# Kernel tuning notes

Measured on AMD Instinct MI355X. Metric: run time of the kernel, lower is better.

The kernel has to match this reference:

```python
import jax, jax.numpy as jnp
import numpy as np

T, B = 64, 512
X, H, Z, A = 1024, 1024, 256, 64


def setup_inputs() -> dict:
    key = jax.random.key(0)
    ks = jax.random.split(key, 24)
    s = 0.02
    n = lambda k, shape: (jax.random.normal(k, shape, dtype=jnp.float32) * s)
    d = {
        "obs_seq": jax.random.normal(ks[0], (T, B, X), dtype=jnp.float32),
        "act_seq": jax.random.normal(ks[1], (T, B, A), dtype=jnp.float32),
        "eps": jax.random.normal(ks[2], (T, B, Z), dtype=jnp.float32),
        # Transition: aggr Linear(z+a -> h), GRUCell(h, h)
        "aggr_W": n(ks[3], (Z + A, H)), "aggr_b": jnp.zeros((H,), jnp.float32),
        "gru_Wih": n(ks[4], (H, 3 * H)), "gru_Whh": n(ks[5], (H, 3 * H)),
        "gru_bih": jnp.zeros((3 * H,), jnp.float32), "gru_bhh": jnp.zeros((3 * H,), jnp.float32),
        # z_q_dist: NormalPredictor(x+h -> hidden h -> z)
        "q_W1": n(ks[6], (X + H, H)), "q_b1": jnp.zeros((H,), jnp.float32),
        "q_Wm": n(ks[7], (H, Z)), "q_bm": jnp.zeros((Z,), jnp.float32),
        "q_Ws": n(ks[8], (H, Z)), "q_bs": jnp.zeros((Z,), jnp.float32),
        # z_p_dist: NormalPredictor(h -> hidden h -> z)
        "p_W1": n(ks[9], (H, H)), "p_b1": jnp.zeros((H,), jnp.float32),
        "p_Wm": n(ks[10], (H, Z)), "p_bm": jnp.zeros((Z,), jnp.float32),
        "p_Ws": n(ks[11], (H, Z)), "p_bs": jnp.zeros((Z,), jnp.float32),
    }
    return d


def _gru_cell(x, h, Wih, Whh, bih, bhh):
    # torch.nn.GRUCell math
    gi = x @ Wih + bih
    gh = h @ Whh + bhh
    i_r, i_z, i_n = jnp.split(gi, 3, axis=-1)
    h_r, h_z, h_n = jnp.split(gh, 3, axis=-1)
    r = jax.nn.sigmoid(i_r + h_r)
    z = jax.nn.sigmoid(i_z + h_z)
    n = jnp.tanh(i_n + r * h_n)
    return (1.0 - z) * n + z * h


def _normal_predictor(x, W1, b1, Wm, bm, Ws, bs):
    hid = jax.nn.elu(x @ W1 + b1)
    loc = hid @ Wm + bm
    scale = jax.nn.softplus(hid @ Ws + bs)
    return loc, scale


def reference(obs_seq, act_seq, eps, aggr_W, aggr_b, gru_Wih, gru_Whh, gru_bih,
              gru_bhh, q_W1, q_b1, q_Wm, q_bm, q_Ws, q_bs, p_W1, p_b1, p_Wm,
              p_bm, p_Ws, p_bs):
    batch = obs_seq.shape[1]
    h0 = jnp.zeros((batch, gru_Whh.shape[0]), dtype=obs_seq.dtype)

    def step(h, inp):
        obs, act, e = inp
        q_loc, q_scale = _normal_predictor(
            jnp.concatenate([obs, h], axis=-1), q_W1, q_b1, q_Wm, q_bm, q_Ws, q_bs)
        z_q = q_loc + q_scale * e  # rsample
        p_loc, p_scale = _normal_predictor(h, p_W1, p_b1, p_Wm, p_bm, p_Ws, p_bs)
        a = jax.nn.elu(jnp.concatenate([z_q, act], axis=-1) @ aggr_W + aggr_b)
        h_new = _gru_cell(a, h, gru_Wih, gru_Whh, gru_bih, gru_bhh)
        return h_new, (h_new, q_loc, q_scale, p_loc, p_scale, z_q)

    _, (bel, q_loc, q_scale, p_loc, p_scale, z_qs) = jax.lax.scan(
        step, h0, (obs_seq, act_seq, eps))
    beliefs = jnp.concatenate([h0[None], bel], axis=0)  # [T+1, B, H]
    return beliefs, (q_loc, q_scale), (p_loc, p_scale), z_qs
```

## Files before the change

### kernel.cpp

```cpp
#include <hip/hip_runtime.h>
#include <hip/hip_bf16.h>
#include <stdint.h>

#define TT 64
#define BB 512
#define XX 1024
#define HH 1024
#define ZZ 256
#define AA 64

typedef __bf16 bf16;
typedef bf16 bf16x8 __attribute__((ext_vector_type(8)));
typedef float f32x4 __attribute__((ext_vector_type(4)));

#define SZ_BEL ((long)(TT + 1) * BB * HH)
#define SZ_TBZ ((long)TT * BB * ZZ)
#define OFF_QL (SZ_BEL)
#define OFF_QS (OFF_QL + SZ_TBZ)
#define OFF_ZQ (OFF_QL + 4 * SZ_TBZ)

#define GLL16(g, l)                                                         \
  __builtin_amdgcn_global_load_lds(                                         \
      (__attribute__((address_space(1))) void*)(g),                         \
      (__attribute__((address_space(3))) void*)(l), 16, 0, 0)

__device__ __forceinline__ float eluf(float x) {
  return x > 0.f ? x : expf(x) - 1.f;
}
__device__ __forceinline__ float splusf(float x) {
  return fmaxf(x, 0.f) + log1pf(expf(-fabsf(x)));
}
__device__ __forceinline__ float sigf(float x) {
  return 1.f / (1.f + expf(-x));
}

struct GArgs {
  const bf16* A; const float* Af; const bf16* A2;
  long lda, lda2; int ksplit;
  const bf16* Bt;
  int M, N, K, t;
  const float *b_q1, *b_p1, *b_ghh, *b_gih;
  const float *b_qm, *b_qs, *b_pm, *b_ps, *b_ag;
  const bf16* obs_pre;
  bf16 *hid_q, *hid_p, *a_buf, *out_bf;
  float *gh, *gi, *dout;
};

template <int BM, int BN, int EPI, bool AF32>
__global__ __launch_bounds__(256) void gemm_k(GArgs g) {
  constexpr int BK = 32;
  constexpr int WTM = BM / 2, WTN = BN / 2;
  constexpr int MR = WTM / 16, NR = WTN / 16;
  constexpr int CA = BM * 4 / 256, CB = BN * 4 / 256;
  __shared__ bf16 sA[BM * BK];
  __shared__ bf16 sB[BN * BK];
  const int nbm = g.M / BM;
  const int bm = blockIdx.x % nbm, bn = blockIdx.x / nbm;
  const int m0 = bm * BM, n0 = bn * BN;
  const int tid = threadIdx.x;
  const int wid = tid >> 6, lane = tid & 63;
  const int wm = wid & 1, wn = wid >> 1;
  const int lr = lane & 15, lk = lane >> 4;

  const bf16* Ap = g.A;
  if (EPI == 2 && n0 >= 512) Ap = g.A2;

  f32x4 acc[MR][NR] = {};

  for (int k0 = 0; k0 < g.K; k0 += BK) {
    __syncthreads();
    if constexpr (AF32) {
#pragma unroll
      for (int i = 0; i < CA; i++) {
        int c = tid + i * 256, row = c >> 2, kc = c & 3;
        const float* s = g.Af + (long)(m0 + row) * g.lda + k0 + kc * 8;
        float4 v0 = *(const float4*)s;
        float4 v1 = *(const float4*)(s + 4);
        bf16x8 p;
        p[0] = (bf16)v0.x; p[1] = (bf16)v0.y; p[2] = (bf16)v0.z; p[3] = (bf16)v0.w;
        p[4] = (bf16)v1.x; p[5] = (bf16)v1.y; p[6] = (bf16)v1.z; p[7] = (bf16)v1.w;
        *(bf16x8*)&sA[c * 8] = p;
      }
    } else {
#pragma unroll
      for (int i = 0; i < CA; i++) {
        int c = tid + i * 256, row = c >> 2, kc = c & 3;
        const bf16* s;
        if (EPI == 3 && k0 >= g.ksplit)
          s = g.A2 + (long)(m0 + row) * g.lda2 + (k0 - g.ksplit) + kc * 8;
        else
          s = Ap + (long)(m0 + row) * g.lda + k0 + kc * 8;
        GLL16(s, &sA[c * 8]);
      }
    }
#pragma unroll
    for (int i = 0; i < CB; i++) {
      int c = tid + i * 256, row = c >> 2, kc = c & 3;
      GLL16(g.Bt + (long)(n0 + row) * g.K + k0 + kc * 8, &sB[c * 8]);
    }
    __syncthreads();
    bf16x8 af[MR];
#pragma unroll
    for (int mi = 0; mi < MR; mi++)
      af[mi] = *(const bf16x8*)&sA[(wm * WTM + mi * 16 + lr) * BK + lk * 8];
#pragma unroll
    for (int nj = 0; nj < NR; nj++) {
      bf16x8 bfr = *(const bf16x8*)&sB[(wn * WTN + nj * 16 + lr) * BK + lk * 8];
#pragma unroll
      for (int mi = 0; mi < MR; mi++)
        acc[mi][nj] = __builtin_amdgcn_mfma_f32_16x16x32_bf16(af[mi], bfr, acc[mi][nj], 0, 0, 0);
    }
  }

#pragma unroll
  for (int mi = 0; mi < MR; mi++) {
#pragma unroll
    for (int nj = 0; nj < NR; nj++) {
#pragma unroll
      for (int r = 0; r < 4; r++) {
        const int row = m0 + wm * WTM + mi * 16 + lk * 4 + r;
        const int col = n0 + wn * WTN + nj * 16 + lr;
        float v = acc[mi][nj][r];
        if constexpr (EPI == 0) {
          g.out_bf[(long)row * g.N + col] = (bf16)v;
        } else if constexpr (EPI == 1) {
          if (col < HH) {
            float x = v + g.b_q1[col] + (float)g.obs_pre[((long)g.t * BB + row) * HH + col];
            g.hid_q[row * HH + col] = (bf16)eluf(x);
          } else if (col < 2 * HH) {
            int j = col - HH;
            g.hid_p[row * HH + j] = (bf16)eluf(v + g.b_p1[j]);
          } else {
            int j = col - 2 * HH;
            g.gh[(long)row * 3 * HH + j] = v + g.b_ghh[j];
          }
        } else if constexpr (EPI == 2) {
          int region = col >> 8, j = col & 255;
          const float* bias = region == 0 ? g.b_qm : region == 1 ? g.b_qs
                            : region == 2 ? g.b_pm : g.b_ps;
          float x = v + bias[j];
          if (region & 1) x = splusf(x);
          g.dout[OFF_QL + (long)region * SZ_TBZ + ((long)g.t * BB + row) * ZZ + j] = x;
        } else if constexpr (EPI == 3) {
          g.a_buf[row * HH + col] = (bf16)eluf(v + g.b_ag[col]);
        } else {
          g.gi[(long)row * 3 * HH + col] = v + g.b_gih[col];
        }
      }
    }
  }
}

__global__ void transpose_cvt(const float* __restrict__ src, bf16* __restrict__ dst,
                              int K, int N, int ld, int k_off) {
  __shared__ float tile[32][33];
  const int nb = blockIdx.x * 32, kb = blockIdx.y * 32;
  const int tx = threadIdx.x, ty = threadIdx.y;
#pragma unroll
  for (int j = 0; j < 32; j += 8)
    tile[ty + j][tx] = src[(long)(kb + ty + j + k_off) * ld + nb + tx];
  __syncthreads();
#pragma unroll
  for (int j = 0; j < 32; j += 8)
    dst[(long)(nb + ty + j) * K + kb + tx] = (bf16)tile[tx][ty + j];
}

__global__ void cvt_bf16(const float* __restrict__ src, bf16* __restrict__ dst, long n) {
  long i = ((long)blockIdx.x * blockDim.x + threadIdx.x) * 4;
  if (i < n) {
    float4 v = *(const float4*)(src + i);
    dst[i] = (bf16)v.x; dst[i + 1] = (bf16)v.y;
    dst[i + 2] = (bf16)v.z; dst[i + 3] = (bf16)v.w;
  }
}

__global__ void init_k(bf16* hbf, float* dout) {
  int i = blockIdx.x * 256 + threadIdx.x;
  hbf[i] = (bf16)0.f;
  dout[i] = 0.f;
}

__global__ void zq_k(const float* __restrict__ eps, float* dout, bf16* zbf, int t) {
  long i = (long)blockIdx.x * 256 + threadIdx.x;
  long o = (long)t * BB * ZZ + i;
  float ql = dout[OFF_QL + o], qs = dout[OFF_QS + o];
  float z = ql + qs * eps[o];
  dout[OFF_ZQ + o] = z;
  zbf[i] = (bf16)z;
}

__global__ void gates_k(const float* __restrict__ gi, const float* __restrict__ gh,
                        bf16* hbf, float* dout, int t) {
  long i = (long)blockIdx.x * 256 + threadIdx.x;
  int m = (int)(i >> 10), j = (int)(i & 1023);
  long b = (long)m * 3 * HH + j;
  float r = sigf(gi[b] + gh[b]);
  float z = sigf(gi[b + HH] + gh[b + HH]);
  float nn = tanhf(gi[b + 2 * HH] + r * gh[b + 2 * HH]);
  float h = (float)hbf[i];
  float hnew = (1.f - z) * nn + z * h;
  hbf[i] = (bf16)hnew;
  dout[(long)(t + 1) * BB * HH + i] = hnew;
}

extern "C" void kernel_launch(void* const* d_in, const int* in_sizes, int n_in,
                              void* d_out, int out_size, void* d_ws, size_t ws_size,
                              hipStream_t stream) {
  const float* obs  = (const float*)d_in[0];
  const float* act  = (const float*)d_in[1];
  const float* eps  = (const float*)d_in[2];
  const float* aggrW = (const float*)d_in[3];
  const float* aggrB = (const float*)d_in[4];
  const float* gWih = (const float*)d_in[5];
  const float* gWhh = (const float*)d_in[6];
  const float* gbih = (const float*)d_in[7];
  const float* gbhh = (const float*)d_in[8];
  const float* qW1  = (const float*)d_in[9];
  const float* qb1  = (const float*)d_in[10];
  const float* qWm  = (const float*)d_in[11];
  const float* qbm  = (const float*)d_in[12];
  const float* qWs  = (const float*)d_in[13];
  const float* qbs  = (const float*)d_in[14];
  const float* pW1  = (const float*)d_in[15];
  const float* pb1  = (const float*)d_in[16];
  const float* pWm  = (const float*)d_in[17];
  const float* pbm  = (const float*)d_in[18];
  const float* pWs  = (const float*)d_in[19];
  const float* pbs  = (const float*)d_in[20];
  float* dout = (float*)d_out;

  char* w = (char*)d_ws;
  size_t off = 0;
  auto alloc = [&](size_t bytes) -> char* {
    char* r = w + off;
    off = (off + bytes + 255) & ~(size_t)255;
    return r;
  };
  bf16* WT_qobs = (bf16*)alloc((size_t)XX * HH * 2);
  bf16* WT_h   = (bf16*)alloc((size_t)5120 * 1024 * 2);
  bf16* WT_k2  = (bf16*)alloc((size_t)1024 * 1024 * 2);
  bf16* WT_ag  = (bf16*)alloc((size_t)1024 * 320 * 2);
  bf16* WT_ih  = (bf16*)alloc((size_t)3072 * 1024 * 2);
  bf16* obs_pre = (bf16*)alloc((size_t)TT * BB * HH * 2);
  bf16* act_bf = (bf16*)alloc((size_t)TT * BB * AA * 2);
  bf16* h_bf   = (bf16*)alloc((size_t)BB * HH * 2);
  bf16* hid_q  = (bf16*)alloc((size_t)BB * HH * 2);
  bf16* hid_p  = (bf16*)alloc((size_t)BB * HH * 2);
  bf16* z_bf   = (bf16*)alloc((size_t)BB * ZZ * 2);
  bf16* a_buf  = (bf16*)alloc((size_t)BB * HH * 2);
  float* gh_f  = (float*)alloc((size_t)BB * 3 * HH * 4);
  float* gi_f  = (float*)alloc((size_t)BB * 3 * HH * 4);
  (void)ws_size; (void)in_sizes; (void)n_in; (void)out_size;

  dim3 tb(32, 8);
  transpose_cvt<<<dim3(32, 32), tb, 0, stream>>>(qW1, WT_qobs, 1024, 1024, 1024, 0);
  transpose_cvt<<<dim3(32, 32), tb, 0, stream>>>(qW1, WT_h, 1024, 1024, 1024, 1024);
  transpose_cvt<<<dim3(32, 32), tb, 0, stream>>>(pW1, WT_h + 1024 * 1024, 1024, 1024, 1024, 0);
  transpose_cvt<<<dim3(96, 32), tb, 0, stream>>>(gWhh, WT_h + 2048 * 1024, 1024, 3072, 3072, 0);
  transpose_cvt<<<dim3(8, 32), tb, 0, stream>>>(qWm, WT_k2, 1024, 256, 256, 0);
  transpose_cvt<<<dim3(8, 32), tb, 0, stream>>>(qWs, WT_k2 + 256 * 1024, 1024, 256, 256, 0);
  transpose_cvt<<<dim3(8, 32), tb, 0, stream>>>(pWm, WT_k2 + 512 * 1024, 1024, 256, 256, 0);
  transpose_cvt<<<dim3(8, 32), tb, 0, stream>>>(pWs, WT_k2 + 768 * 1024, 1024, 256, 256, 0);
  transpose_cvt<<<dim3(32, 10), tb, 0, stream>>>(aggrW, WT_ag, 320, 1024, 1024, 0);
  transpose_cvt<<<dim3(96, 32), tb, 0, stream>>>(gWih, WT_ih, 1024, 3072, 3072, 0);
  cvt_bf16<<<TT * BB * AA / 4 / 256, 256, 0, stream>>>(act, act_bf, (long)TT * BB * AA);
  init_k<<<BB * HH / 256, 256, 0, stream>>>(h_bf, dout);

  GArgs g{};
  g.b_q1 = qb1; g.b_p1 = pb1; g.b_ghh = gbhh; g.b_gih = gbih;
  g.b_qm = qbm; g.b_qs = qbs; g.b_pm = pbm; g.b_ps = pbs; g.b_ag = aggrB;
  g.obs_pre = obs_pre; g.hid_q = hid_q; g.hid_p = hid_p; g.a_buf = a_buf;
  g.gh = gh_f; g.gi = gi_f; g.dout = dout;

  {
    GArgs a = g;
    a.Af = obs; a.lda = XX; a.Bt = WT_qobs;
    a.M = TT * BB; a.N = HH; a.K = XX; a.out_bf = obs_pre;
    gemm_k<128, 128, 0, true><<<(TT * BB / 128) * (HH / 128), 256, 0, stream>>>(a);
  }

  for (int t = 0; t < TT; ++t) {
    {
      GArgs a = g; a.t = t;
      a.A = h_bf; a.lda = HH; a.Bt = WT_h;
      a.M = BB; a.N = 5120; a.K = HH;
      gemm_k<64, 128, 1, false><<<(BB / 64) * (5120 / 128), 256, 0, stream>>>(a);
    }
    {
      GArgs a = g; a.t = t;
      a.A = hid_q; a.A2 = hid_p; a.lda = HH; a.Bt = WT_k2;
      a.M = BB; a.N = 1024; a.K = HH;
      gemm_k<64, 128, 2, false><<<(BB / 64) * (1024 / 128), 256, 0, stream>>>(a);
    }
    zq_k<<<BB * ZZ / 256, 256, 0, stream>>>(eps, dout, z_bf, t);
    {
      GArgs a = g; a.t = t;
      a.A = z_bf; a.lda = ZZ;
      a.A2 = act_bf + (size_t)t * BB * AA; a.lda2 = AA; a.ksplit = ZZ;
      a.Bt = WT_ag; a.M = BB; a.N = 1024; a.K = ZZ + AA;
      gemm_k<64, 128, 3, false><<<(BB / 64) * (1024 / 128), 256, 0, stream>>>(a);
    }
    {
      GArgs a = g; a.t = t;
      a.A = a_buf; a.lda = HH; a.Bt = WT_ih;
      a.M = BB; a.N = 3 * HH; a.K = HH;
      gemm_k<64, 128, 4, false><<<(BB / 64) * (3 * HH / 128), 256, 0, stream>>>(a);
    }
    gates_k<<<BB * HH / 256, 256, 0, stream>>>(gi_f, gh_f, h_bf, dout, t);
  }
}
```

Measured before the change: 6.584 ms.

## Hoist prior-network GEMMs out of the recurrence and fuse z_q and GRU gate epilogues

The prior network p(h) depends only on beliefs and does not feed back into the scan, so it is moved out of the per-timestep loop. It now runs as two large batched GEMMs over all T*B rows after the recurrence, and its hidden buffer reuses the obs_pre workspace, which is no longer needed by then. The q loc/scale GEMM is fused with the reparameterized sample in a dedicated kernel, and the GRU input GEMM is fused with the gate nonlinearities, which removes the zq and gates kernels and the gi buffer round-trip. The fused per-step kernels launch only 16 and 128 blocks, which may underfill the GPU on the sequential critical path.

```diff
diff --git a/kernel.cpp b/kernel.cpp
--- a/kernel.cpp
+++ b/kernel.cpp
@@ -17,6 +17,8 @@
 #define SZ_TBZ ((long)TT * BB * ZZ)
 #define OFF_QL (SZ_BEL)
 #define OFF_QS (OFF_QL + SZ_TBZ)
+#define OFF_PL (OFF_QL + 2 * SZ_TBZ)
+#define OFF_PS (OFF_QL + 3 * SZ_TBZ)
 #define OFF_ZQ (OFF_QL + 4 * SZ_TBZ)
 
 #define GLL16(g, l)                                                         \
@@ -39,11 +41,10 @@
   long lda, lda2; int ksplit;
   const bf16* Bt;
   int M, N, K, t;
-  const float *b_q1, *b_p1, *b_ghh, *b_gih;
-  const float *b_qm, *b_qs, *b_pm, *b_ps, *b_ag;
+  const float *b_q1, *b_ghh, *b_ag, *b_p1, *b_pm, *b_ps;
   const bf16* obs_pre;
-  bf16 *hid_q, *hid_p, *a_buf, *out_bf;
-  float *gh, *gi, *dout;
+  bf16 *hid_q, *a_buf, *out_bf;
+  float *gh, *dout;
 };
 
 template <int BM, int BN, int EPI, bool AF32>
@@ -62,9 +63,6 @@
   const int wm = wid & 1, wn = wid >> 1;
   const int lr = lane & 15, lk = lane >> 4;
 
-  const bf16* Ap = g.A;
-  if (EPI == 2 && n0 >= 512) Ap = g.A2;
-
   f32x4 acc[MR][NR] = {};
 
   for (int k0 = 0; k0 < g.K; k0 += BK) {
@@ -89,7 +87,7 @@
         if (EPI == 3 && k0 >= g.ksplit)
           s = g.A2 + (long)(m0 + row) * g.lda2 + (k0 - g.ksplit) + kc * 8;
         else
-          s = Ap + (long)(m0 + row) * g.lda + k0 + kc * 8;
+          s = g.A + (long)(m0 + row) * g.lda + k0 + kc * 8;
         GLL16(s, &sA[c * 8]);
       }
     }
@@ -127,25 +125,159 @@
           if (col < HH) {
             float x = v + g.b_q1[col] + (float)g.obs_pre[((long)g.t * BB + row) * HH + col];
             g.hid_q[row * HH + col] = (bf16)eluf(x);
-          } else if (col < 2 * HH) {
+          } else {
             int j = col - HH;
-            g.hid_p[row * HH + j] = (bf16)eluf(v + g.b_p1[j]);
-          } else {
-            int j = col - 2 * HH;
             g.gh[(long)row * 3 * HH + j] = v + g.b_ghh[j];
           }
-        } else if constexpr (EPI == 2) {
-          int region = col >> 8, j = col & 255;
-          const float* bias = region == 0 ? g.b_qm : region == 1 ? g.b_qs
-                            : region == 2 ? g.b_pm : g.b_ps;
-          float x = v + bias[j];
-          if (region & 1) x = splusf(x);
-          g.dout[OFF_QL + (long)region * SZ_TBZ + ((long)g.t * BB + row) * ZZ + j] = x;
         } else if constexpr (EPI == 3) {
           g.a_buf[row * HH + col] = (bf16)eluf(v + g.b_ag[col]);
+        } else if constexpr (EPI == 5) {
+          g.out_bf[(long)row * g.N + col] = (bf16)eluf(v + g.b_p1[col]);
         } else {
-          g.gi[(long)row * 3 * HH + col] = v + g.b_gih[col];
+          int region = col >> 8, j = col & 255;
+          float x = v + (region ? g.b_ps[j] : g.b_pm[j]);
+          if (region) x = splusf(x);
+          g.dout[(region ? OFF_PS : OFF_PL) + (long)row * ZZ + j] = x;
         }
+      }
+    }
+  }
+}
+
+struct QZArgs {
+  const bf16* A; const bf16* Bt2;
+  const float *b_qm, *b_qs; const float* eps;
+  float* dout; bf16* z_bf; int t;
+};
+__global__ __launch_bounds__(256) void qz_gemm(QZArgs g) {
+  constexpr int BK = 32;
+  __shared__ bf16 sA[64 * BK];
+  __shared__ bf16 sB[256 * BK];
+  const int bm = blockIdx.x & 7, bn = blockIdx.x >> 3;
+  const int m0 = bm * 64, n0 = bn * 128;
+  const int tid = threadIdx.x;
+  const int wid = tid >> 6, lane = tid & 63;
+  const int wm = wid & 1, wn = wid >> 1;
+  const int lr = lane & 15, lk = lane >> 4;
+
+  f32x4 accL[2][4] = {}, accS[2][4] = {};
+
+  for (int k0 = 0; k0 < HH; k0 += BK) {
+    __syncthreads();
+    {
+      int c = tid, row = c >> 2, kc = c & 3;
+      GLL16(g.A + (long)(m0 + row) * HH + k0 + kc * 8, &sA[c * 8]);
+    }
+#pragma unroll
+    for (int i = 0; i < 4; i++) {
+      int c = tid + i * 256, row = c >> 2, kc = c & 3;
+      int grow = (row < 128) ? (n0 + row) : (256 + n0 + (row - 128));
+      GLL16(g.Bt2 + (long)grow * HH + k0 + kc * 8, &sB[c * 8]);
+    }
+    __syncthreads();
+    bf16x8 af[2];
+#pragma unroll
+    for (int mi = 0; mi < 2; mi++)
+      af[mi] = *(const bf16x8*)&sA[(wm * 32 + mi * 16 + lr) * BK + lk * 8];
+#pragma unroll
+    for (int nj = 0; nj < 4; nj++) {
+      bf16x8 bL = *(const bf16x8*)&sB[(wn * 64 + nj * 16 + lr) * BK + lk * 8];
+      bf16x8 bS = *(const bf16x8*)&sB[(128 + wn * 64 + nj * 16 + lr) * BK + lk * 8];
+#pragma unroll
+      for (int mi = 0; mi < 2; mi++) {
+        accL[mi][nj] = __builtin_amdgcn_mfma_f32_16x16x32_bf16(af[mi], bL, accL[mi][nj], 0, 0, 0);
+        accS[mi][nj] = __builtin_amdgcn_mfma_f32_16x16x32_bf16(af[mi], bS, accS[mi][nj], 0, 0, 0);
+      }
+    }
+  }
+
+#pragma unroll
+  for (int mi = 0; mi < 2; mi++) {
+#pragma unroll
+    for (int nj = 0; nj < 4; nj++) {
+#pragma unroll
+      for (int r = 0; r < 4; r++) {
+        const int row = m0 + wm * 32 + mi * 16 + lk * 4 + r;
+        const int j = n0 + wn * 64 + nj * 16 + lr;
+        long o = ((long)g.t * BB + row) * ZZ + j;
+        float loc = accL[mi][nj][r] + g.b_qm[j];
+        float sc = splusf(accS[mi][nj][r] + g.b_qs[j]);
+        float z = loc + sc * g.eps[o];
+        g.dout[OFF_QL + o] = loc;
+        g.dout[OFF_QS + o] = sc;
+        g.dout[OFF_ZQ + o] = z;
+        g.z_bf[row * ZZ + j] = (bf16)z;
+      }
+    }
+  }
+}
+
+struct GRUArgs {
+  const bf16* A; const bf16* Bt;
+  const float* b_gih; const float* gh;
+  bf16* h_bf; float* dout; int t;
+};
+__global__ __launch_bounds__(256) void gru_gemm(GRUArgs g) {
+  constexpr int BK = 32;
+  __shared__ bf16 sA[64 * BK];
+  __shared__ bf16 sB[192 * BK];
+  const int bm = blockIdx.x & 7, bn = blockIdx.x >> 3;
+  const int m0 = bm * 64, n0 = bn * 64;
+  const int tid = threadIdx.x;
+  const int wid = tid >> 6, lane = tid & 63;
+  const int wm = wid & 1, wn = wid >> 1;
+  const int lr = lane & 15, lk = lane >> 4;
+
+  f32x4 acc[2][3][2] = {};
+
+  for (int k0 = 0; k0 < HH; k0 += BK) {
+    __syncthreads();
+    {
+      int c = tid, row = c >> 2, kc = c & 3;
+      GLL16(g.A + (long)(m0 + row) * HH + k0 + kc * 8, &sA[c * 8]);
+    }
+#pragma unroll
+    for (int i = 0; i < 3; i++) {
+      int c = tid + i * 256, row = c >> 2, kc = c & 3;
+      int gate = row >> 6, jr = row & 63;
+      GLL16(g.Bt + (long)(gate * HH + n0 + jr) * HH + k0 + kc * 8, &sB[c * 8]);
+    }
+    __syncthreads();
+    bf16x8 af[2];
+#pragma unroll
+    for (int mi = 0; mi < 2; mi++)
+      af[mi] = *(const bf16x8*)&sA[(wm * 32 + mi * 16 + lr) * BK + lk * 8];
+#pragma unroll
+    for (int gt = 0; gt < 3; gt++) {
+#pragma unroll
+      for (int nj = 0; nj < 2; nj++) {
+        bf16x8 bfr = *(const bf16x8*)&sB[(gt * 64 + wn * 32 + nj * 16 + lr) * BK + lk * 8];
+#pragma unroll
+        for (int mi = 0; mi < 2; mi++)
+          acc[mi][gt][nj] = __builtin_amdgcn_mfma_f32_16x16x32_bf16(af[mi], bfr, acc[mi][gt][nj], 0, 0, 0);
+      }
+    }
+  }
+
+#pragma unroll
+  for (int mi = 0; mi < 2; mi++) {
+#pragma unroll
+    for (int nj = 0; nj < 2; nj++) {
+#pragma unroll
+      for (int r = 0; r < 4; r++) {
+        const int row = m0 + wm * 32 + mi * 16 + lk * 4 + r;
+        const int j = n0 + wn * 32 + nj * 16 + lr;
+        const long gb = (long)row * 3 * HH + j;
+        float gir = acc[mi][0][nj][r] + g.b_gih[j];
+        float giz = acc[mi][1][nj][r] + g.b_gih[HH + j];
+        float gin = acc[mi][2][nj][r] + g.b_gih[2 * HH + j];
+        float rr = sigf(gir + g.gh[gb]);
+        float zz = sigf(giz + g.gh[gb + HH]);
+        float nn = tanhf(gin + rr * g.gh[gb + 2 * HH]);
+        float h = (float)g.h_bf[row * HH + j];
+        float hn = (1.f - zz) * nn + zz * h;
+        g.h_bf[row * HH + j] = (bf16)hn;
+        g.dout[(long)(g.t + 1) * BB * HH + (long)row * HH + j] = hn;
       }
     }
   }
@@ -178,29 +310,6 @@
   int i = blockIdx.x * 256 + threadIdx.x;
   hbf[i] = (bf16)0.f;
   dout[i] = 0.f;
-}
-
-__global__ void zq_k(const float* __restrict__ eps, float* dout, bf16* zbf, int t) {
-  long i = (long)blockIdx.x * 256 + threadIdx.x;
-  long o = (long)t * BB * ZZ + i;
-  float ql = dout[OFF_QL + o], qs = dout[OFF_QS + o];
-  float z = ql + qs * eps[o];
-  dout[OFF_ZQ + o] = z;
-  zbf[i] = (bf16)z;
-}
-
-__global__ void gates_k(const float* __restrict__ gi, const float* __restrict__ gh,
-                        bf16* hbf, float* dout, int t) {
-  long i = (long)blockIdx.x * 256 + threadIdx.x;
-  int m = (int)(i >> 10), j = (int)(i & 1023);
-  long b = (long)m * 3 * HH + j;
-  float r = sigf(gi[b] + gh[b]);
-  float z = sigf(gi[b + HH] + gh[b + HH]);
-  float nn = tanhf(gi[b + 2 * HH] + r * gh[b + 2 * HH]);
-  float h = (float)hbf[i];
-  float hnew = (1.f - z) * nn + z * h;
-  hbf[i] = (bf16)hnew;
-  dout[(long)(t + 1) * BB * HH + i] = hnew;
 }
 
 extern "C" void kernel_launch(void* const* d_in, const int* in_sizes, int n_in,
@@ -237,40 +346,41 @@
     return r;
   };
   bf16* WT_qobs = (bf16*)alloc((size_t)XX * HH * 2);
-  bf16* WT_h   = (bf16*)alloc((size_t)5120 * 1024 * 2);
-  bf16* WT_k2  = (bf16*)alloc((size_t)1024 * 1024 * 2);
+  bf16* WT_h   = (bf16*)alloc((size_t)4096 * 1024 * 2);
+  bf16* WT_qh  = (bf16*)alloc((size_t)512 * 1024 * 2);
   bf16* WT_ag  = (bf16*)alloc((size_t)1024 * 320 * 2);
   bf16* WT_ih  = (bf16*)alloc((size_t)3072 * 1024 * 2);
+  bf16* WT_p1  = (bf16*)alloc((size_t)1024 * 1024 * 2);
+  bf16* WT_ph  = (bf16*)alloc((size_t)512 * 1024 * 2);
   bf16* obs_pre = (bf16*)alloc((size_t)TT * BB * HH * 2);
+  bf16* p_hid  = obs_pre;
   bf16* act_bf = (bf16*)alloc((size_t)TT * BB * AA * 2);
   bf16* h_bf   = (bf16*)alloc((size_t)BB * HH * 2);
   bf16* hid_q  = (bf16*)alloc((size_t)BB * HH * 2);
-  bf16* hid_p  = (bf16*)alloc((size_t)BB * HH * 2);
   bf16* z_bf   = (bf16*)alloc((size_t)BB * ZZ * 2);
   bf16* a_buf  = (bf16*)alloc((size_t)BB * HH * 2);
   float* gh_f  = (float*)alloc((size_t)BB * 3 * HH * 4);
-  float* gi_f  = (float*)alloc((size_t)BB * 3 * HH * 4);
   (void)ws_size; (void)in_sizes; (void)n_in; (void)out_size;
 
   dim3 tb(32, 8);
   transpose_cvt<<<dim3(32, 32), tb, 0, stream>>>(qW1, WT_qobs, 1024, 1024, 1024, 0);
   transpose_cvt<<<dim3(32, 32), tb, 0, stream>>>(qW1, WT_h, 1024, 1024, 1024, 1024);
-  transpose_cvt<<<dim3(32, 32), tb, 0, stream>>>(pW1, WT_h + 1024 * 1024, 1024, 1024, 1024, 0);
-  transpose_cvt<<<dim3(96, 32), tb, 0, stream>>>(gWhh, WT_h + 2048 * 1024, 1024, 3072, 3072, 0);
-  transpose_cvt<<<dim3(8, 32), tb, 0, stream>>>(qWm, WT_k2, 1024, 256, 256, 0);
-  transpose_cvt<<<dim3(8, 32), tb, 0, stream>>>(qWs, WT_k2 + 256 * 1024, 1024, 256, 256, 0);
-  transpose_cvt<<<dim3(8, 32), tb, 0, stream>>>(pWm, WT_k2 + 512 * 1024, 1024, 256, 256, 0);
-  transpose_cvt<<<dim3(8, 32), tb, 0, stream>>>(pWs, WT_k2 + 768 * 1024, 1024, 256, 256, 0);
+  transpose_cvt<<<dim3(96, 32), tb, 0, stream>>>(gWhh, WT_h + 1024 * 1024, 1024, 3072, 3072, 0);
+  transpose_cvt<<<dim3(8, 32), tb, 0, stream>>>(qWm, WT_qh, 1024, 256, 256, 0);
+  transpose_cvt<<<dim3(8, 32), tb, 0, stream>>>(qWs, WT_qh + 256 * 1024, 1024, 256, 256, 0);
   transpose_cvt<<<dim3(32, 10), tb, 0, stream>>>(aggrW, WT_ag, 320, 1024, 1024, 0);
   transpose_cvt<<<dim3(96, 32), tb, 0, stream>>>(gWih, WT_ih, 1024, 3072, 3072, 0);
+  transpose_cvt<<<dim3(32, 32), tb, 0, stream>>>(pW1, WT_p1, 1024, 1024, 1024, 0);
+  transpose_cvt<<<dim3(8, 32), tb, 0, stream>>>(pWm, WT_ph, 1024, 256, 256, 0);
+  transpose_cvt<<<dim3(8, 32), tb, 0, stream>>>(pWs, WT_ph + 256 * 1024, 1024, 256, 256, 0);
   cvt_bf16<<<TT * BB * AA / 4 / 256, 256, 0, stream>>>(act, act_bf, (long)TT * BB * AA);
   init_k<<<BB * HH / 256, 256, 0, stream>>>(h_bf, dout);
 
   GArgs g{};
-  g.b_q1 = qb1; g.b_p1 = pb1; g.b_ghh = gbhh; g.b_gih = gbih;
-  g.b_qm = qbm; g.b_qs = qbs; g.b_pm = pbm; g.b_ps = pbs; g.b_ag = aggrB;
-  g.obs_pre = obs_pre; g.hid_q = hid_q; g.hid_p = hid_p; g.a_buf = a_buf;
-  g.gh = gh_f; g.gi = gi_f; g.dout = dout;
+  g.b_q1 = qb1; g.b_ghh = gbhh; g.b_ag = aggrB; g.b_p1 = pb1;
+  g.b_pm = pbm; g.b_ps = pbs;
+  g.obs_pre = obs_pre; g.hid_q = hid_q; g.a_buf = a_buf;
+  g.gh = gh_f; g.dout = dout;
 
   {
     GArgs a = g;
@@ -283,16 +393,13 @@
     {
       GArgs a = g; a.t = t;
       a.A = h_bf; a.lda = HH; a.Bt = WT_h;
-      a.M = BB; a.N = 5120; a.K = HH;
-      gemm_k<64, 128, 1, false><<<(BB / 64) * (5120 / 128), 256, 0, stream>>>(a);
-    }
-    {
-      GArgs a = g; a.t = t;
-      a.A = hid_q; a.A2 = hid_p; a.lda = HH; a.Bt = WT_k2;
-      a.M = BB; a.N = 1024; a.K = HH;
-      gemm_k<64, 128, 2, false><<<(BB / 64) * (1024 / 128), 256, 0, stream>>>(a);
-    }
-    zq_k<<<BB * ZZ / 256, 256, 0, stream>>>(eps, dout, z_bf, t);
+      a.M = BB; a.N = 4096; a.K = HH;
+      gemm_k<64, 128, 1, false><<<(BB / 64) * (4096 / 128), 256, 0, stream>>>(a);
+    }
+    {
+      QZArgs a{hid_q, WT_qh, qbm, qbs, eps, dout, z_bf, t};
+      qz_gemm<<<8 * 2, 256, 0, stream>>>(a);
+    }
     {
       GArgs a = g; a.t = t;
       a.A = z_bf; a.lda = ZZ;
@@ -301,11 +408,21 @@
       gemm_k<64, 128, 3, false><<<(BB / 64) * (1024 / 128), 256, 0, stream>>>(a);
     }
     {
-      GArgs a = g; a.t = t;
-      a.A = a_buf; a.lda = HH; a.Bt = WT_ih;
-      a.M = BB; a.N = 3 * HH; a.K = HH;
-      gemm_k<64, 128, 4, false><<<(BB / 64) * (3 * HH / 128), 256, 0, stream>>>(a);
-    }
-    gates_k<<<BB * HH / 256, 256, 0, stream>>>(gi_f, gh_f, h_bf, dout, t);
-  }
-}
+      GRUArgs a{a_buf, WT_ih, gbih, gh_f, h_bf, dout, t};
+      gru_gemm<<<8 * 16, 256, 0, stream>>>(a);
+    }
+  }
+
+  {
+    GArgs a = g;
+    a.Af = dout; a.lda = HH; a.Bt = WT_p1;
+    a.M = TT * BB; a.N = HH; a.K = HH; a.out_bf = p_hid;
+    gemm_k<128, 128, 5, true><<<(TT * BB / 128) * (HH / 128), 256, 0, stream>>>(a);
+  }
+  {
+    GArgs a = g;
+    a.A = p_hid; a.lda = HH; a.Bt = WT_ph;
+    a.M = TT * BB; a.N = 512; a.K = HH;
+    gemm_k<128, 128, 6, false><<<(TT * BB / 128) * (512 / 128), 256, 0, stream>>>(a);
+  }
+}
```

After: 7.323 ms. +11.2%, slower.
